# Performance work log

Measured on AMD Instinct MI355X. Metric: run time of the kernel, lower is better.

Reference implementation:

```python
import jax, jax.numpy as jnp
import numpy as np

NUM_HEADS = 8

def setup_inputs() -> dict:
    key = jax.random.key(0)
    ks = jax.random.split(key, 6)
    B, nW, F_W, ED = 8, 64, 128, 512
    x = jax.random.normal(ks[0], (B * nW, F_W, ED), dtype=jnp.float32)
    adj_mask = jax.random.normal(ks[1], (B, NUM_HEADS, F_W, F_W), dtype=jnp.float32)
    qkv_w = jax.random.normal(ks[2], (ED, 3 * ED), dtype=jnp.float32) * (ED ** -0.5)
    qkv_b = jax.random.normal(ks[3], (3 * ED,), dtype=jnp.float32) * 0.02
    proj_w = jax.random.normal(ks[4], (ED, ED), dtype=jnp.float32) * (ED ** -0.5)
    proj_b = jax.random.normal(ks[5], (ED,), dtype=jnp.float32) * 0.02
    return {"x": x, "adj_mask": adj_mask, "qkv_w": qkv_w, "qkv_b": qkv_b,
            "proj_w": proj_w, "proj_b": proj_b, "B": B, "nW": nW}

def reference(x, adj_mask, qkv_w, qkv_b, proj_w, proj_b, B, nW):
    B_nW, F_W, ED = x.shape
    H = NUM_HEADS
    hd = ED // H
    scale = hd ** -0.5
    # qkv projection: [B_nW, F_W, 3, H, hd]
    qkv = (x @ qkv_w + qkv_b).reshape(B_nW, F_W, 3, H, hd)
    qkv = jnp.transpose(qkv, (2, 0, 3, 1, 4))  # [3, B_nW, H, F_W, hd]
    q, k, v = qkv[0], qkv[1], qkv[2]
    attn = jnp.einsum('bhqd,bhkd->bhqk', q * scale, k)  # [B_nW, H, F_W, F_W]
    # additive adjacency mask, broadcast over windows
    attn = attn.reshape(B, nW, H, F_W, F_W) + adj_mask[:, None]
    attn = attn.reshape(B_nW, H, F_W, F_W)
    attn = jax.nn.softmax(attn, axis=-1)
    out = jnp.einsum('bhqk,bhkd->bhqd', attn, v)  # [B_nW, H, F_W, hd]
    out = jnp.transpose(out, (0, 2, 1, 3)).reshape(B_nW, F_W, ED)
    return out @ proj_w + proj_b
```

## Files before the change

### kernel.cpp

```cpp
#include <hip/hip_runtime.h>

typedef __bf16 bf16_t;
typedef __bf16 bf16x8 __attribute__((ext_vector_type(8)));
typedef float f32x4 __attribute__((ext_vector_type(4)));

#define MFMA16(a, b, c) __builtin_amdgcn_mfma_f32_16x16x32_bf16(a, b, c, 0, 0, 0)

#define F_W 128
#define ED 512
#define NH 8
#define HD 64
#define B_NW 512
#define NTOK 65536

typedef const __attribute__((address_space(1))) void gvoid_t;
typedef __attribute__((address_space(3))) void lvoid_t;
__device__ __forceinline__ void gload16(const void* g, void* l) {
    __builtin_amdgcn_global_load_lds((gvoid_t*)g, (lvoid_t*)l, 16, 0, 0);
}

__global__ __launch_bounds__(256) void prep_kernel(
    const float* __restrict__ qkv_w,
    const float* __restrict__ proj_w,
    bf16_t* __restrict__ qkv_wt,
    bf16_t* __restrict__ proj_wt) {
    int idx = blockIdx.x * 256 + threadIdx.x;
    if (idx < 1536 * 512) {
        int n = idx >> 9, k = idx & 511;
        qkv_wt[idx] = (bf16_t)qkv_w[k * 1536 + n];
    }
    if (idx < 512 * 512) {
        int n = idx >> 9, k = idx & 511;
        proj_wt[idx] = (bf16_t)proj_w[k * 512 + n];
    }
}

__global__ __launch_bounds__(256, 4) void qkv_gemm_kernel(
    const float* __restrict__ x,
    const bf16_t* __restrict__ qkv_wt,
    const float* __restrict__ qkv_b,
    bf16_t* qk_ws,
    bf16_t* vt_ws) {
    __shared__ __align__(16) char sm[24576];
    float*  x_s = (float*)sm;
    bf16_t* w_s = (bf16_t*)(sm + 16384);
    bf16_t* tb  = (bf16_t*)sm;

    const int tid = threadIdx.x;
    const int wave = tid >> 6, lane = tid & 63;
    const int lrow = lane & 15, lgrp = lane >> 4;
    const int bid = blockIdx.x;
    const int idx = bid >> 3;
    const int mt_l = idx / 12;
    const int nt = idx - mt_l * 12;
    const int mtile = (bid & 7) * 64 + mt_l;
    const size_t m0 = (size_t)mtile * 128;
    const int n0 = nt * 128;

    const int xrow_l = lane >> 3;
    const int xcol_l = ((lane & 7) * 4) ^ ((xrow_l & 7) << 2);
    const int wrow_l = lane >> 2;
    const int wcol_l = ((lane & 3) * 8) ^ ((wrow_l & 3) << 3);

    f32x4 acc[2][8];
#pragma unroll
    for (int mf = 0; mf < 2; ++mf)
#pragma unroll
        for (int nf = 0; nf < 8; ++nf) acc[mf][nf] = (f32x4)0.0f;

    for (int kc = 0; kc < 16; ++kc) {
        const int k0 = kc * 32;
        __syncthreads();
#pragma unroll
        for (int i = 0; i < 4; ++i) {
            int c = wave * 4 + i;
            gload16(x + (m0 + c * 8 + xrow_l) * 512 + k0 + xcol_l, x_s + c * 256);
        }
#pragma unroll
        for (int i = 0; i < 2; ++i) {
            int c = wave * 2 + i;
            int n = n0 + c * 16 + wrow_l;
            gload16(qkv_wt + (size_t)n * 512 + k0 + wcol_l, w_s + c * 512);
        }
        __syncthreads();

        bf16x8 a[2], b[8];
#pragma unroll
        for (int mf = 0; mf < 2; ++mf) {
            int row = wave * 32 + mf * 16 + lrow;
            int sw = (row & 7) << 2;
            const float* px = x_s + row * 32;
            f32x4 lo = *(const f32x4*)(px + ((lgrp * 8) ^ sw));
            f32x4 hi = *(const f32x4*)(px + ((lgrp * 8 + 4) ^ sw));
            a[mf] = bf16x8{(bf16_t)lo[0], (bf16_t)lo[1], (bf16_t)lo[2], (bf16_t)lo[3],
                           (bf16_t)hi[0], (bf16_t)hi[1], (bf16_t)hi[2], (bf16_t)hi[3]};
        }
#pragma unroll
        for (int nf = 0; nf < 8; ++nf) {
            int row = nf * 16 + lrow;
            b[nf] = *(const bf16x8*)(w_s + row * 32 + ((lgrp * 8) ^ ((row & 3) << 3)));
        }
#pragma unroll
        for (int mf = 0; mf < 2; ++mf)
#pragma unroll
            for (int nf = 0; nf < 8; ++nf)
                acc[mf][nf] = MFMA16(a[mf], b[nf], acc[mf][nf]);
    }

    if (nt < 8) {
        const float scale = (nt < 4) ? 0.125f : 1.0f;
#pragma unroll
        for (int nf = 0; nf < 8; ++nf) {
            int col = n0 + nf * 16 + lrow;
            float bv = qkv_b[col];
#pragma unroll
            for (int mf = 0; mf < 2; ++mf)
#pragma unroll
                for (int j = 0; j < 4; ++j) {
                    int r = wave * 32 + mf * 16 + lgrp * 4 + j;
                    qk_ws[(m0 + r) * 1024 + col] =
                        (bf16_t)((acc[mf][nf][j] + bv) * scale);
                }
        }
    } else {
#pragma unroll
        for (int hh = 0; hh < 2; ++hh) {
            int h = (nt - 8) * 2 + hh;
            __syncthreads();
#pragma unroll
            for (int mf = 0; mf < 2; ++mf)
#pragma unroll
                for (int nfl = 0; nfl < 4; ++nfl) {
                    int nf = hh * 4 + nfl;
                    int d = nfl * 16 + lrow;
                    float bv = qkv_b[n0 + hh * 64 + d];
#pragma unroll
                    for (int j = 0; j < 4; ++j) {
                        int r = wave * 32 + mf * 16 + lgrp * 4 + j;
                        tb[r * 72 + d] = (bf16_t)(acc[mf][nf][j] + bv);
                    }
                }
            __syncthreads();
            {
                int d = tid & 63;
                int kh = tid >> 6;
                bf16_t* outp = vt_ws + ((size_t)(mtile * 8 + h) * 64 + d) * 128 + kh * 32;
#pragma unroll
                for (int o = 0; o < 4; ++o) {
                    bf16x8 v;
#pragma unroll
                    for (int e = 0; e < 8; ++e)
                        v[e] = tb[(kh * 32 + o * 8 + e) * 72 + d];
                    *(bf16x8*)(outp + o * 8) = v;
                }
            }
        }
    }
}

__global__ __launch_bounds__(512, 4) void attn_kernel(
    bf16_t* qk_ws,
    const bf16_t* __restrict__ vt_ws,
    const float* __restrict__ adj) {
    __shared__ __align__(16) char sm[32768];
    bf16_t* k_lds  = (bf16_t*)sm;
    bf16_t* vt_lds = (bf16_t*)(sm + 16384);
    bf16_t* pbuf   = (bf16_t*)sm;

    const int tid = threadIdx.x;
    const int wave = tid >> 6, lane = tid & 63;
    const int lrow = lane & 15, lgrp = lane >> 4;
    const int bid = blockIdx.x;
    const int w = (bid & 7) * 64 + (bid >> 6);
    const int h = (bid >> 3) & 7;
    const int bidx = bid & 7;

    bf16_t* qrow = qk_ws + (size_t)w * 128 * 1024;

    {
        const int krow_l = lane >> 3;
        const int kcol_l = ((lane & 7) * 8) ^ ((krow_l & 7) << 3);
#pragma unroll
        for (int i = 0; i < 2; ++i) {
            int c = wave * 2 + i;
            gload16(qrow + (size_t)(c * 8 + krow_l) * 1024 + 512 + h * 64 + kcol_l,
                    k_lds + c * 512);
        }
    }
    {
        const bf16_t* vtb = vt_ws + (size_t)(w * 8 + h) * 64 * 128;
        const int vrow_l = lane >> 4;
#pragma unroll
        for (int i = 0; i < 2; ++i) {
            int c = wave * 2 + i;
            int d = c * 4 + vrow_l;
            int vcol = ((lane & 15) * 8) ^ ((d & 7) << 3);
            gload16(vtb + (size_t)d * 128 + vcol, vt_lds + c * 512);
        }
    }
    bf16x8 aq[2];
    {
        int row = wave * 16 + lrow;
#pragma unroll
        for (int kb = 0; kb < 2; ++kb)
            aq[kb] = *(const bf16x8*)(qrow + (size_t)row * 1024 + h * 64 + kb * 32 + lgrp * 8);
    }
    __syncthreads();

    f32x4 sacc[8];
#pragma unroll
    for (int nf = 0; nf < 8; ++nf) sacc[nf] = (f32x4)0.0f;
#pragma unroll
    for (int kb = 0; kb < 2; ++kb) {
        bf16x8 b[8];
#pragma unroll
        for (int nf = 0; nf < 8; ++nf) {
            int row = nf * 16 + lrow;
            b[nf] = *(const bf16x8*)(k_lds + row * 64 + ((kb * 32 + lgrp * 8) ^ ((row & 7) << 3)));
        }
#pragma unroll
        for (int nf = 0; nf < 8; ++nf)
            sacc[nf] = MFMA16(aq[kb], b[nf], sacc[nf]);
    }

    const float* mbase = adj + ((size_t)(bidx * NH + h)) * F_W * F_W;
#pragma unroll
    for (int j = 0; j < 4; ++j) {
        int row = wave * 16 + lgrp * 4 + j;
        const float* mrow = mbase + (size_t)row * F_W;
        float mx = -1e30f;
#pragma unroll
        for (int nf = 0; nf < 8; ++nf) {
            sacc[nf][j] += mrow[nf * 16 + lrow];
            mx = fmaxf(mx, sacc[nf][j]);
        }
#pragma unroll
        for (int d = 1; d < 16; d <<= 1) mx = fmaxf(mx, __shfl_xor(mx, d));
        float sum = 0.f;
#pragma unroll
        for (int nf = 0; nf < 8; ++nf) {
            float p = exp2f((sacc[nf][j] - mx) * 1.44269504f);
            sacc[nf][j] = p;
            sum += p;
        }
#pragma unroll
        for (int d = 1; d < 16; d <<= 1) sum += __shfl_xor(sum, d);
        float r = 1.0f / sum;
#pragma unroll
        for (int nf = 0; nf < 8; ++nf) sacc[nf][j] *= r;
    }
    __syncthreads();

    f32x4 oacc[4];
#pragma unroll
    for (int nf = 0; nf < 4; ++nf) oacc[nf] = (f32x4)0.0f;

#pragma unroll
    for (int kb = 0; kb < 4; ++kb) {
#pragma unroll
        for (int nn = 0; nn < 2; ++nn) {
            int nf = kb * 2 + nn;
            int kk = nn * 16 + lrow;
#pragma unroll
            for (int j = 0; j < 4; ++j) {
                int r = wave * 16 + lgrp * 4 + j;
                pbuf[r * 40 + kk] = (bf16_t)(sacc[nf][j]);
            }
        }
        __syncthreads();
        bf16x8 a = *(const bf16x8*)(pbuf + (wave * 16 + lrow) * 40 + lgrp * 8);
        bf16x8 b[4];
#pragma unroll
        for (int nf = 0; nf < 4; ++nf) {
            int d = nf * 16 + lrow;
            b[nf] = *(const bf16x8*)(vt_lds + d * 128 + ((kb * 32 + lgrp * 8) ^ ((d & 7) << 3)));
        }
#pragma unroll
        for (int nf = 0; nf < 4; ++nf)
            oacc[nf] = MFMA16(a, b[nf], oacc[nf]);
        __syncthreads();
    }

#pragma unroll
    for (int nf = 0; nf < 4; ++nf) {
        int ocol = h * 64 + nf * 16 + lrow;
#pragma unroll
        for (int j = 0; j < 4; ++j) {
            int r = wave * 16 + lgrp * 4 + j;
            qrow[(size_t)r * 1024 + ocol] = (bf16_t)oacc[nf][j];
        }
    }
}

__global__ __launch_bounds__(256) void proj_kernel(
    const bf16_t* __restrict__ a_g,
    const bf16_t* __restrict__ bt_g,
    const float* __restrict__ bias,
    float* __restrict__ out) {
    __shared__ __align__(16) bf16_t sm_[8192];
    bf16_t* a_s = sm_;
    bf16_t* b_s = sm_ + 4096;
    const int tid = threadIdx.x;
    const int wave = tid >> 6, lane = tid & 63;
    const int lrow = lane & 15, lgrp = lane >> 4;
    const int bid = blockIdx.x;
    const int mtile = (bid & 7) * 64 + (bid >> 5);
    const int ntile = (bid >> 3) & 3;
    const size_t m0 = (size_t)mtile * 128;
    const int n0 = ntile * 128;
    const int wrow_l = lane >> 2;
    const int wcol_l = ((lane & 3) * 8) ^ ((wrow_l & 3) << 3);

    f32x4 acc[2][8];
#pragma unroll
    for (int mf = 0; mf < 2; ++mf)
#pragma unroll
        for (int nf = 0; nf < 8; ++nf) acc[mf][nf] = (f32x4)0.0f;

    for (int kc = 0; kc < 16; ++kc) {
        const int k0 = kc * 32;
        __syncthreads();
#pragma unroll
        for (int i = 0; i < 2; ++i) {
            int c = wave * 2 + i;
            gload16(a_g + (m0 + c * 16 + wrow_l) * 1024 + k0 + wcol_l, a_s + c * 512);
            gload16(bt_g + (size_t)(n0 + c * 16 + wrow_l) * 512 + k0 + wcol_l, b_s + c * 512);
        }
        __syncthreads();
        bf16x8 a[2], b[8];
#pragma unroll
        for (int mf = 0; mf < 2; ++mf) {
            int row = wave * 32 + mf * 16 + lrow;
            a[mf] = *(const bf16x8*)(a_s + row * 32 + ((lgrp * 8) ^ ((row & 3) << 3)));
        }
#pragma unroll
        for (int nf = 0; nf < 8; ++nf) {
            int row = nf * 16 + lrow;
            b[nf] = *(const bf16x8*)(b_s + row * 32 + ((lgrp * 8) ^ ((row & 3) << 3)));
        }
#pragma unroll
        for (int mf = 0; mf < 2; ++mf)
#pragma unroll
            for (int nf = 0; nf < 8; ++nf)
                acc[mf][nf] = MFMA16(a[mf], b[nf], acc[mf][nf]);
    }

#pragma unroll
    for (int nf = 0; nf < 8; ++nf) {
        int col = n0 + nf * 16 + lrow;
        float bv = bias[col];
#pragma unroll
        for (int mf = 0; mf < 2; ++mf)
#pragma unroll
            for (int j = 0; j < 4; ++j) {
                size_t row = m0 + wave * 32 + mf * 16 + lgrp * 4 + j;
                out[row * 512 + col] = acc[mf][nf][j] + bv;
            }
    }
}

extern "C" void kernel_launch(void* const* d_in, const int* in_sizes, int n_in,
                              void* d_out, int out_size, void* d_ws, size_t ws_size,
                              hipStream_t stream) {
    const float* x      = (const float*)d_in[0];
    const float* adj    = (const float*)d_in[1];
    const float* qkv_w  = (const float*)d_in[2];
    const float* qkv_b  = (const float*)d_in[3];
    const float* proj_w = (const float*)d_in[4];
    const float* proj_b = (const float*)d_in[5];
    float* out = (float*)d_out;

    bf16_t* qk_ws   = (bf16_t*)d_ws;
    bf16_t* vt_ws   = qk_ws + (size_t)NTOK * 1024;
    bf16_t* qkv_wt  = vt_ws + (size_t)4096 * 64 * 128;
    bf16_t* proj_wt = qkv_wt + 1536 * 512;

    prep_kernel<<<3072, 256, 0, stream>>>(qkv_w, proj_w, qkv_wt, proj_wt);
    qkv_gemm_kernel<<<6144, 256, 0, stream>>>(x, qkv_wt, qkv_b, qk_ws, vt_ws);
    attn_kernel<<<4096, 512, 0, stream>>>(qk_ws, vt_ws, adj);
    proj_kernel<<<2048, 256, 0, stream>>>(qk_ws, proj_wt, proj_b, out);
}
```

Measured before the change: 330.7 us.

## Pre-convert x to bf16 and use 2x2 wave tiling in QKV and proj GEMMs

Adds a pass that converts x from fp32 to bf16 into the output buffer, used as scratch, so the QKV GEMM loads half the bytes per tile and skips in-loop fp32-to-bf16 conversion. Both GEMMs change from 4 waves each covering 32 rows by 128 columns to a 2x2 wave grid of 64x64 subtiles, which cuts LDS fragment reads per MFMA. The swizzle is changed to suit the new read pattern, and proj gets a launch-bounds occupancy hint. The extra conversion pass writes and rereads 64MB of bf16, which costs bandwidth against the GEMM savings.

```diff
diff --git a/kernel.cpp b/kernel.cpp
--- a/kernel.cpp
+++ b/kernel.cpp
@@ -18,6 +18,8 @@
 __device__ __forceinline__ void gload16(const void* g, void* l) {
     __builtin_amdgcn_global_load_lds((gvoid_t*)g, (lvoid_t*)l, 16, 0, 0);
 }
+
+__device__ __forceinline__ int swz32(int row) { return ((row >> 1) & 3) << 3; }
 
 __global__ __launch_bounds__(256) void prep_kernel(
     const float* __restrict__ qkv_w,
@@ -35,20 +37,31 @@
     }
 }
 
+__global__ __launch_bounds__(256) void prep_x_kernel(
+    const float* __restrict__ x, bf16_t* __restrict__ xbf) {
+    size_t i = ((size_t)blockIdx.x * 256 + threadIdx.x) * 8;
+    float4 v0 = *(const float4*)(x + i);
+    float4 v1 = *(const float4*)(x + i + 4);
+    bf16x8 o = {(bf16_t)v0.x, (bf16_t)v0.y, (bf16_t)v0.z, (bf16_t)v0.w,
+                (bf16_t)v1.x, (bf16_t)v1.y, (bf16_t)v1.z, (bf16_t)v1.w};
+    *(bf16x8*)(xbf + i) = o;
+}
+
 __global__ __launch_bounds__(256, 4) void qkv_gemm_kernel(
-    const float* __restrict__ x,
+    const bf16_t* __restrict__ xbf,
     const bf16_t* __restrict__ qkv_wt,
     const float* __restrict__ qkv_b,
     bf16_t* qk_ws,
     bf16_t* vt_ws) {
-    __shared__ __align__(16) char sm[24576];
-    float*  x_s = (float*)sm;
-    bf16_t* w_s = (bf16_t*)(sm + 16384);
+    __shared__ __align__(16) char sm[18432];
+    bf16_t* x_s = (bf16_t*)sm;
+    bf16_t* w_s = (bf16_t*)(sm + 8192);
     bf16_t* tb  = (bf16_t*)sm;
 
     const int tid = threadIdx.x;
     const int wave = tid >> 6, lane = tid & 63;
     const int lrow = lane & 15, lgrp = lane >> 4;
+    const int wm = wave >> 1, wn = wave & 1;
     const int bid = blockIdx.x;
     const int idx = bid >> 3;
     const int mt_l = idx / 12;
@@ -57,67 +70,60 @@
     const size_t m0 = (size_t)mtile * 128;
     const int n0 = nt * 128;
 
-    const int xrow_l = lane >> 3;
-    const int xcol_l = ((lane & 7) * 4) ^ ((xrow_l & 7) << 2);
-    const int wrow_l = lane >> 2;
-    const int wcol_l = ((lane & 3) * 8) ^ ((wrow_l & 3) << 3);
-
-    f32x4 acc[2][8];
-#pragma unroll
-    for (int mf = 0; mf < 2; ++mf)
-#pragma unroll
-        for (int nf = 0; nf < 8; ++nf) acc[mf][nf] = (f32x4)0.0f;
+    const int row16 = lane >> 2;
+    const int scol = ((lane & 3) * 8) ^ swz32(row16);
+
+    f32x4 acc[4][4];
+#pragma unroll
+    for (int mf = 0; mf < 4; ++mf)
+#pragma unroll
+        for (int nf = 0; nf < 4; ++nf) acc[mf][nf] = (f32x4)0.0f;
 
     for (int kc = 0; kc < 16; ++kc) {
         const int k0 = kc * 32;
         __syncthreads();
 #pragma unroll
-        for (int i = 0; i < 4; ++i) {
-            int c = wave * 4 + i;
-            gload16(x + (m0 + c * 8 + xrow_l) * 512 + k0 + xcol_l, x_s + c * 256);
-        }
-#pragma unroll
-        for (int i = 0; i < 2; ++i) {
-            int c = wave * 2 + i;
-            int n = n0 + c * 16 + wrow_l;
-            gload16(qkv_wt + (size_t)n * 512 + k0 + wcol_l, w_s + c * 512);
-        }
-        __syncthreads();
-
-        bf16x8 a[2], b[8];
-#pragma unroll
-        for (int mf = 0; mf < 2; ++mf) {
-            int row = wave * 32 + mf * 16 + lrow;
-            int sw = (row & 7) << 2;
-            const float* px = x_s + row * 32;
-            f32x4 lo = *(const f32x4*)(px + ((lgrp * 8) ^ sw));
-            f32x4 hi = *(const f32x4*)(px + ((lgrp * 8 + 4) ^ sw));
-            a[mf] = bf16x8{(bf16_t)lo[0], (bf16_t)lo[1], (bf16_t)lo[2], (bf16_t)lo[3],
-                           (bf16_t)hi[0], (bf16_t)hi[1], (bf16_t)hi[2], (bf16_t)hi[3]};
-        }
-#pragma unroll
-        for (int nf = 0; nf < 8; ++nf) {
-            int row = nf * 16 + lrow;
-            b[nf] = *(const bf16x8*)(w_s + row * 32 + ((lgrp * 8) ^ ((row & 3) << 3)));
-        }
-#pragma unroll
-        for (int mf = 0; mf < 2; ++mf)
-#pragma unroll
-            for (int nf = 0; nf < 8; ++nf)
+        for (int i = 0; i < 2; ++i) {
+            int c = wave * 2 + i;
+            gload16(xbf + (m0 + c * 16 + row16) * 512 + k0 + scol, x_s + c * 512);
+        }
+#pragma unroll
+        for (int i = 0; i < 2; ++i) {
+            int c = wave * 2 + i;
+            gload16(qkv_wt + (size_t)(n0 + c * 16 + row16) * 512 + k0 + scol,
+                    w_s + c * 512);
+        }
+        __syncthreads();
+
+        bf16x8 a[4], b[4];
+#pragma unroll
+        for (int mf = 0; mf < 4; ++mf) {
+            int row = wm * 64 + mf * 16 + lrow;
+            a[mf] = *(const bf16x8*)(x_s + row * 32 + ((lgrp * 8) ^ swz32(row)));
+        }
+#pragma unroll
+        for (int nf = 0; nf < 4; ++nf) {
+            int rw = wn * 64 + nf * 16 + lrow;
+            b[nf] = *(const bf16x8*)(w_s + rw * 32 + ((lgrp * 8) ^ swz32(rw)));
+        }
+#pragma unroll
+        for (int mf = 0; mf < 4; ++mf)
+#pragma unroll
+            for (int nf = 0; nf < 4; ++nf)
                 acc[mf][nf] = MFMA16(a[mf], b[nf], acc[mf][nf]);
     }
 
     if (nt < 8) {
         const float scale = (nt < 4) ? 0.125f : 1.0f;
 #pragma unroll
-        for (int nf = 0; nf < 8; ++nf) {
-            int col = n0 + nf * 16 + lrow;
+        for (int nf = 0; nf < 4; ++nf) {
+            int col = n0 + wn * 64 + nf * 16 + lrow;
             float bv = qkv_b[col];
 #pragma unroll
-            for (int mf = 0; mf < 2; ++mf)
+            for (int mf = 0; mf < 4; ++mf)
 #pragma unroll
                 for (int j = 0; j < 4; ++j) {
-                    int r = wave * 32 + mf * 16 + lgrp * 4 + j;
+                    int r = wm * 64 + mf * 16 + lgrp * 4 + j;
                     qk_ws[(m0 + r) * 1024 + col] =
                         (bf16_t)((acc[mf][nf][j] + bv) * scale);
                 }
@@ -127,19 +133,20 @@
         for (int hh = 0; hh < 2; ++hh) {
             int h = (nt - 8) * 2 + hh;
             __syncthreads();
-#pragma unroll
-            for (int mf = 0; mf < 2; ++mf)
-#pragma unroll
-                for (int nfl = 0; nfl < 4; ++nfl) {
-                    int nf = hh * 4 + nfl;
-                    int d = nfl * 16 + lrow;
+            if (wn == hh) {
+#pragma unroll
+                for (int nf = 0; nf < 4; ++nf) {
+                    int d = nf * 16 + lrow;
                     float bv = qkv_b[n0 + hh * 64 + d];
 #pragma unroll
-                    for (int j = 0; j < 4; ++j) {
-                        int r = wave * 32 + mf * 16 + lgrp * 4 + j;
-                        tb[r * 72 + d] = (bf16_t)(acc[mf][nf][j] + bv);
-                    }
+                    for (int mf = 0; mf < 4; ++mf)
+#pragma unroll
+                        for (int j = 0; j < 4; ++j) {
+                            int r = wm * 64 + mf * 16 + lgrp * 4 + j;
+                            tb[r * 72 + d] = (bf16_t)(acc[mf][nf][j] + bv);
+                        }
                 }
+            }
             __syncthreads();
             {
                 int d = tid & 63;
@@ -292,7 +299,7 @@
     }
 }
 
-__global__ __launch_bounds__(256) void proj_kernel(
+__global__ __launch_bounds__(256, 4) void proj_kernel(
     const bf16_t* __restrict__ a_g,
     const bf16_t* __restrict__ bt_g,
     const float* __restrict__ bias,
@@ -303,19 +310,20 @@
     const int tid = threadIdx.x;
     const int wave = tid >> 6, lane = tid & 63;
     const int lrow = lane & 15, lgrp = lane >> 4;
+    const int wm = wave >> 1, wn = wave & 1;
     const int bid = blockIdx.x;
     const int mtile = (bid & 7) * 64 + (bid >> 5);
     const int ntile = (bid >> 3) & 3;
     const size_t m0 = (size_t)mtile * 128;
     const int n0 = ntile * 128;
-    const int wrow_l = lane >> 2;
-    const int wcol_l = ((lane & 3) * 8) ^ ((wrow_l & 3) << 3);
-
-    f32x4 acc[2][8];
-#pragma unroll
-    for (int mf = 0; mf < 2; ++mf)
-#pragma unroll
-        for (int nf = 0; nf < 8; ++nf) acc[mf][nf] = (f32x4)0.0f;
+    const int row16 = lane >> 2;
+    const int scol = ((lane & 3) * 8) ^ swz32(row16);
+
+    f32x4 acc[4][4];
+#pragma unroll
+    for (int mf = 0; mf < 4; ++mf)
+#pragma unroll
+        for (int nf = 0; nf < 4; ++nf) acc[mf][nf] = (f32x4)0.0f;
 
     for (int kc = 0; kc < 16; ++kc) {
         const int k0 = kc * 32;
@@ -323,37 +331,37 @@
 #pragma unroll
         for (int i = 0; i < 2; ++i) {
             int c = wave * 2 + i;
-            gload16(a_g + (m0 + c * 16 + wrow_l) * 1024 + k0 + wcol_l, a_s + c * 512);
-            gload16(bt_g + (size_t)(n0 + c * 16 + wrow_l) * 512 + k0 + wcol_l, b_s + c * 512);
-        }
-        __syncthreads();
-        bf16x8 a[2], b[8];
-#pragma unroll
-        for (int mf = 0; mf < 2; ++mf) {
-            int row = wave * 32 + mf * 16 + lrow;
-            a[mf] = *(const bf16x8*)(a_s + row * 32 + ((lgrp * 8) ^ ((row & 3) << 3)));
-        }
-#pragma unroll
-        for (int nf = 0; nf < 8; ++nf) {
-            int row = nf * 16 + lrow;
-            b[nf] = *(const bf16x8*)(b_s + row * 32 + ((lgrp * 8) ^ ((row & 3) << 3)));
-        }
-#pragma unroll
-        for (int mf = 0; mf < 2; ++mf)
-#pragma unroll
-            for (int nf = 0; nf < 8; ++nf)
+            gload16(a_g + (m0 + c * 16 + row16) * 1024 + k0 + scol, a_s + c * 512);
+            gload16(bt_g + (size_t)(n0 + c * 16 + row16) * 512 + k0 + scol, b_s + c * 512);
+        }
+        __syncthreads();
+        bf16x8 a[4], b[4];
+#pragma unroll
+        for (int mf = 0; mf < 4; ++mf) {
+            int row = wm * 64 + mf * 16 + lrow;
+            a[mf] = *(const bf16x8*)(a_s + row * 32 + ((lgrp * 8) ^ swz32(row)));
+        }
+#pragma unroll
+        for (int nf = 0; nf < 4; ++nf) {
+            int rw = wn * 64 + nf * 16 + lrow;
+            b[nf] = *(const bf16x8*)(b_s + rw * 32 + ((lgrp * 8) ^ swz32(rw)));
+        }
+#pragma unroll
+        for (int mf = 0; mf < 4; ++mf)
+#pragma unroll
+            for (int nf = 0; nf < 4; ++nf)
                 acc[mf][nf] = MFMA16(a[mf], b[nf], acc[mf][nf]);
     }
 
 #pragma unroll
-    for (int nf = 0; nf < 8; ++nf) {
-        int col = n0 + nf * 16 + lrow;
+    for (int nf = 0; nf < 4; ++nf) {
+        int col = n0 + wn * 64 + nf * 16 + lrow;
         float bv = bias[col];
 #pragma unroll
-        for (int mf = 0; mf < 2; ++mf)
+        for (int mf = 0; mf < 4; ++mf)
 #pragma unroll
             for (int j = 0; j < 4; ++j) {
-                size_t row = m0 + wave * 32 + mf * 16 + lgrp * 4 + j;
+                size_t row = m0 + wm * 64 + mf * 16 + lgrp * 4 + j;
                 out[row * 512 + col] = acc[mf][nf][j] + bv;
             }
     }
@@ -374,9 +382,11 @@
     bf16_t* vt_ws   = qk_ws + (size_t)NTOK * 1024;
     bf16_t* qkv_wt  = vt_ws + (size_t)4096 * 64 * 128;
     bf16_t* proj_wt = qkv_wt + 1536 * 512;
+    bf16_t* xbf = (bf16_t*)d_out;
 
     prep_kernel<<<3072, 256, 0, stream>>>(qkv_w, proj_w, qkv_wt, proj_wt);
-    qkv_gemm_kernel<<<6144, 256, 0, stream>>>(x, qkv_wt, qkv_b, qk_ws, vt_ws);
+    prep_x_kernel<<<NTOK * ED / 8 / 256, 256, 0, stream>>>(x, xbf);
+    qkv_gemm_kernel<<<6144, 256, 0, stream>>>(xbf, qkv_wt, qkv_b, qk_ws, vt_ws);
     attn_kernel<<<4096, 512, 0, stream>>>(qk_ws, vt_ws, adj);
     proj_kernel<<<2048, 256, 0, stream>>>(qk_ws, proj_wt, proj_b, out);
 }
```

After: 317.2 us. 4.1% less time.
